# Kernel tuning notes

Hardware: AMD Instinct MI355X
Metric: run time of the kernel (lower is better)

## Reference

```python
import jax, jax.numpy as jnp
import numpy as np

OUTPUT_DIM = 512
INPUT_DIM = 64
BATCH = 131072


def setup_inputs() -> dict:
    key = jax.random.key(0)
    k1, k2, k3, k4 = jax.random.split(key, 4)
    D = INPUT_DIM + OUTPUT_DIM
    X = jax.random.normal(k1, (BATCH, OUTPUT_DIM), dtype=jnp.float32)
    c = jax.random.normal(k2, (BATCH, INPUT_DIM), dtype=jnp.float32)
    PA = jax.random.normal(k3, (OUTPUT_DIM, D), dtype=jnp.float32) * 0.05
    PB = jax.random.normal(k4, (OUTPUT_DIM, D), dtype=jnp.float32) * 0.05
    return {"X": X, "c": c, "PA": PA, "PB": PB}


def reference(X, c, PA, PB):
    # x = cat(c, X) : [B, D] with D = INPUT_DIM + OUTPUT_DIM
    x = jnp.concatenate([c, X], axis=1)
    D = INPUT_DIM + OUTPUT_DIM
    mask = (jnp.arange(D)[None, :] < (INPUT_DIM + jnp.arange(OUTPUT_DIM))[:, None]).astype(x.dtype)
    A = x @ (PA * mask).T  # [B, OUTPUT_DIM], A[:, i] = pa[i] @ x[:, :INPUT_DIM+i]
    Bv = x @ (PB * mask).T  # [B, OUTPUT_DIM]
    z = X * jnp.exp(A) + Bv  # [B, OUTPUT_DIM]
    log_det = jnp.sum(A, axis=1)  # [B]
    return z, log_det
```

## Files before the change

kernel.cpp:

```cpp
#include <hip/hip_runtime.h>
#include <hip/hip_bf16.h>
#include <stdint.h>

#define N_OUT 512
#define N_IN 64
#define D_TOT 576
#define BM 32
#define ROW_BYTES (D_TOT * 2)
#define NWAVES 4

typedef __attribute__((ext_vector_type(8))) short short8_t;
typedef __attribute__((ext_vector_type(4))) float f32x4;
typedef unsigned short u16;

__device__ __forceinline__ u16 f2bf(float f) {
    __hip_bfloat16 h = __float2bfloat16(f);
    return *reinterpret_cast<u16*>(&h);
}
__device__ __forceinline__ float bf2f(u16 u) {
    union { uint32_t u; float f; } v;
    v.u = ((uint32_t)u) << 16;
    return v.f;
}

__global__ void prep_weights_kernel(const float* __restrict__ PA,
                                    const float* __restrict__ PB,
                                    u16* __restrict__ WA,
                                    u16* __restrict__ WB) {
    const int col = blockIdx.x;
    const int lim = N_IN + col;
    const float* pa = PA + (size_t)col * D_TOT;
    const float* pb = PB + (size_t)col * D_TOT;
    for (int k = threadIdx.x; k < D_TOT; k += blockDim.x) {
        int kk = k >> 5, lg = (k >> 3) & 3, j = k & 7;
        size_t dst = ((size_t)(kk * 4 + lg) * N_OUT + col) * 8 + j;
        bool valid = (k < lim);
        WA[dst] = valid ? f2bf(pa[k]) : (u16)0;
        WB[dst] = valid ? f2bf(pb[k]) : (u16)0;
    }
}

__global__ __launch_bounds__(256)
void maf_main_kernel(const float* __restrict__ X,
                     const float* __restrict__ Cc,
                     const u16* __restrict__ WA,
                     const u16* __restrict__ WB,
                     float* __restrict__ Z,
                     float* __restrict__ LD) {
    extern __shared__ char smem[];
    char* xt = smem;
    float* ldsum = (float*)(smem + BM * ROW_BYTES);

    const int tid = threadIdx.x;
    const int r0 = blockIdx.x * BM;

    {
        int row = tid >> 3, cc = tid & 7;
        const float* src = Cc + (size_t)(r0 + row) * N_IN + cc * 8;
        f32x4 v0 = __builtin_nontemporal_load((const f32x4*)src);
        f32x4 v1 = __builtin_nontemporal_load((const f32x4*)(src + 4));
        short8_t p;
        p[0] = (short)f2bf(v0[0]); p[1] = (short)f2bf(v0[1]);
        p[2] = (short)f2bf(v0[2]); p[3] = (short)f2bf(v0[3]);
        p[4] = (short)f2bf(v1[0]); p[5] = (short)f2bf(v1[1]);
        p[6] = (short)f2bf(v1[2]); p[7] = (short)f2bf(v1[3]);
        int addr = (row * ROW_BYTES + cc * 16) ^ ((row & 7) << 4);
        *(short8_t*)(xt + addr) = p;
    }
    #pragma unroll
    for (int i = 0; i < 8; ++i) {
        int id = tid + i * 256;
        int row = id >> 6, xc = id & 63;
        const float* src = X + (size_t)(r0 + row) * N_OUT + xc * 8;
        f32x4 v0 = __builtin_nontemporal_load((const f32x4*)src);
        f32x4 v1 = __builtin_nontemporal_load((const f32x4*)(src + 4));
        short8_t p;
        p[0] = (short)f2bf(v0[0]); p[1] = (short)f2bf(v0[1]);
        p[2] = (short)f2bf(v0[2]); p[3] = (short)f2bf(v0[3]);
        p[4] = (short)f2bf(v1[0]); p[5] = (short)f2bf(v1[1]);
        p[6] = (short)f2bf(v1[2]); p[7] = (short)f2bf(v1[3]);
        int addr = (row * ROW_BYTES + (8 + xc) * 16) ^ ((row & 7) << 4);
        *(short8_t*)(xt + addr) = p;
    }
    __syncthreads();

    const int wid = tid >> 6;
    const int lane = tid & 63;
    const int lr = lane & 15;
    const int lg = lane >> 4;

    float part[2][4];
    #pragma unroll
    for (int m = 0; m < 2; ++m)
        #pragma unroll
        for (int j = 0; j < 4; ++j) part[m][j] = 0.0f;

    const int groups[4] = { wid, 7 - wid, 8 + wid, 15 - wid };

    #pragma unroll
    for (int gi = 0; gi < 4; ++gi) {
        const int g = groups[gi];
        const int c0 = g << 5;
        const int ksteps = 3 + g;

        f32x4 accA[2][2], accB[2][2];
        #pragma unroll
        for (int m = 0; m < 2; ++m)
            #pragma unroll
            for (int n = 0; n < 2; ++n) {
                accA[m][n] = (f32x4)(0.0f);
                accB[m][n] = (f32x4)(0.0f);
            }

        #pragma unroll 3
        for (int kk = 0; kk < ksteps; ++kk) {
            const int kb = kk * 64 + lg * 16;
            short8_t a[2];
            #pragma unroll
            for (int m = 0; m < 2; ++m) {
                int row = (m << 4) + lr;
                int addr = (row * ROW_BYTES + kb) ^ ((row & 7) << 4);
                a[m] = *(const short8_t*)(xt + addr);
            }
            short8_t ba[2], bb[2];
            const size_t wbase = (size_t)((kk << 2) + lg) * N_OUT + c0 + lr;
            #pragma unroll
            for (int n = 0; n < 2; ++n) {
                size_t off = (wbase + (n << 4)) * 8;
                ba[n] = *(const short8_t*)(WA + off);
                bb[n] = *(const short8_t*)(WB + off);
            }
            #pragma unroll
            for (int m = 0; m < 2; ++m) {
                #pragma unroll
                for (int n = 0; n < 2; ++n) {
                    accA[m][n] = __builtin_amdgcn_mfma_f32_16x16x32_bf16(a[m], ba[n], accA[m][n], 0, 0, 0);
                    accB[m][n] = __builtin_amdgcn_mfma_f32_16x16x32_bf16(a[m], bb[n], accB[m][n], 0, 0, 0);
                }
            }
        }

        #pragma unroll
        for (int m = 0; m < 2; ++m) {
            #pragma unroll
            for (int n = 0; n < 2; ++n) {
                int col = c0 + (n << 4) + lr;
                #pragma unroll
                for (int j = 0; j < 4; ++j) {
                    int row = (m << 4) + (lg << 2) + j;
                    float Av = accA[m][n][j];
                    float Bv = accB[m][n][j];
                    int xaddr = (row * ROW_BYTES + (N_IN + col) * 2) ^ ((row & 7) << 4);
                    float Xf = bf2f(*(const u16*)(xt + xaddr));
                    float zv = Xf * __expf(Av) + Bv;
                    __builtin_nontemporal_store(zv, &Z[(size_t)(r0 + row) * N_OUT + col]);
                    part[m][j] += Av;
                }
            }
        }
    }

    #pragma unroll
    for (int m = 0; m < 2; ++m) {
        #pragma unroll
        for (int j = 0; j < 4; ++j) {
            float v = part[m][j];
            v += __shfl_xor(v, 1);
            v += __shfl_xor(v, 2);
            v += __shfl_xor(v, 4);
            v += __shfl_xor(v, 8);
            if (lr == 0) ldsum[(wid << 5) + (m << 4) + (lg << 2) + j] = v;
        }
    }
    __syncthreads();
    if (tid < BM) {
        float s = 0.0f;
        #pragma unroll
        for (int w = 0; w < NWAVES; ++w) s += ldsum[(w << 5) + tid];
        LD[(size_t)r0 + tid] = s;
    }
}

extern "C" void kernel_launch(void* const* d_in, const int* in_sizes, int n_in,
                              void* d_out, int out_size, void* d_ws, size_t ws_size,
                              hipStream_t stream) {
    const float* X  = (const float*)d_in[0];
    const float* Cc = (const float*)d_in[1];
    const float* PA = (const float*)d_in[2];
    const float* PB = (const float*)d_in[3];

    u16* WA = (u16*)d_ws;
    u16* WB = WA + (size_t)N_OUT * D_TOT;

    float* Z  = (float*)d_out;
    const size_t batch = (size_t)in_sizes[0] / N_OUT;
    float* LD = Z + batch * N_OUT;

    prep_weights_kernel<<<N_OUT, 256, 0, stream>>>(PA, PB, WA, WB);

    const size_t lds_bytes = (size_t)BM * ROW_BYTES + NWAVES * BM * sizeof(float);
    const int grid = (int)(batch / BM);
    maf_main_kernel<<<grid, 256, lds_bytes, stream>>>(X, Cc, WA, WB, Z, LD);
}
```

Measured before the change: 216.4 us.

## Pair column groups per wave to share A-fragment loads across two MFMA chains

Each wave now processes two column groups at once (a short and a long triangular group), reusing the same LDS A-fragments across both groups during the shared k-steps and then finishing the longer group alone. This roughly halves LDS reads of the activation tile and gives more independent MFMA chains for latency hiding. It doubles accumulator register use, which may lower occupancy. The epilogue also switches from nontemporal stores to plain stores for Z.

```diff
diff --git a/kernel.cpp b/kernel.cpp
--- a/kernel.cpp
+++ b/kernel.cpp
@@ -40,6 +40,31 @@
     }
 }
 
+__device__ __forceinline__ void epilogue_group(const char* xt,
+                                               float* __restrict__ Z,
+                                               int r0, int c0, int lr, int lg,
+                                               const f32x4 accE[2][2],
+                                               const f32x4 accV[2][2],
+                                               float part[2][4]) {
+    #pragma unroll
+    for (int m = 0; m < 2; ++m) {
+        #pragma unroll
+        for (int n = 0; n < 2; ++n) {
+            int col = c0 + (n << 4) + lr;
+            #pragma unroll
+            for (int j = 0; j < 4; ++j) {
+                int row = (m << 4) + (lg << 2) + j;
+                float Av = accE[m][n][j];
+                float Bv = accV[m][n][j];
+                int xaddr = (row * ROW_BYTES + (N_IN + col) * 2) ^ ((row & 7) << 4);
+                float Xf = bf2f(*(const u16*)(xt + xaddr));
+                Z[(size_t)(r0 + row) * N_OUT + col] = Xf * __expf(Av) + Bv;
+                part[m][j] += Av;
+            }
+        }
+    }
+}
+
 __global__ __launch_bounds__(256)
 void maf_main_kernel(const float* __restrict__ X,
                      const float* __restrict__ Cc,
@@ -95,25 +120,27 @@
         #pragma unroll
         for (int j = 0; j < 4; ++j) part[m][j] = 0.0f;
 
-    const int groups[4] = { wid, 7 - wid, 8 + wid, 15 - wid };
-
-    #pragma unroll
-    for (int gi = 0; gi < 4; ++gi) {
-        const int g = groups[gi];
-        const int c0 = g << 5;
-        const int ksteps = 3 + g;
-
-        f32x4 accA[2][2], accB[2][2];
+    #pragma unroll
+    for (int pi = 0; pi < 2; ++pi) {
+        const int g0 = (pi == 0) ? wid : 7 - wid;
+        const int g1 = (pi == 0) ? 15 - wid : 8 + wid;
+        const int ks0 = 3 + g0;
+        const int ks1 = 3 + g1;
+        const int c00 = g0 << 5;
+        const int c01 = g1 << 5;
+
+        f32x4 accE0[2][2], accV0[2][2], accE1[2][2], accV1[2][2];
         #pragma unroll
         for (int m = 0; m < 2; ++m)
             #pragma unroll
             for (int n = 0; n < 2; ++n) {
-                accA[m][n] = (f32x4)(0.0f);
-                accB[m][n] = (f32x4)(0.0f);
-            }
-
-        #pragma unroll 3
-        for (int kk = 0; kk < ksteps; ++kk) {
+                accE0[m][n] = (f32x4)(0.0f); accV0[m][n] = (f32x4)(0.0f);
+                accE1[m][n] = (f32x4)(0.0f); accV1[m][n] = (f32x4)(0.0f);
+            }
+
+        int kk = 0;
+        #pragma unroll 2
+        for (; kk < ks0; ++kk) {
             const int kb = kk * 64 + lg * 16;
             short8_t a[2];
             #pragma unroll
@@ -122,42 +149,58 @@
                 int addr = (row * ROW_BYTES + kb) ^ ((row & 7) << 4);
                 a[m] = *(const short8_t*)(xt + addr);
             }
-            short8_t ba[2], bb[2];
-            const size_t wbase = (size_t)((kk << 2) + lg) * N_OUT + c0 + lr;
+            const size_t wrow = (size_t)((kk << 2) + lg) * N_OUT + lr;
+            short8_t e0[2], v0[2], e1[2], v1[2];
             #pragma unroll
             for (int n = 0; n < 2; ++n) {
-                size_t off = (wbase + (n << 4)) * 8;
-                ba[n] = *(const short8_t*)(WA + off);
-                bb[n] = *(const short8_t*)(WB + off);
+                size_t o0 = (wrow + c00 + (n << 4)) * 8;
+                size_t o1 = (wrow + c01 + (n << 4)) * 8;
+                e0[n] = *(const short8_t*)(WA + o0);
+                v0[n] = *(const short8_t*)(WB + o0);
+                e1[n] = *(const short8_t*)(WA + o1);
+                v1[n] = *(const short8_t*)(WB + o1);
             }
             #pragma unroll
             for (int m = 0; m < 2; ++m) {
                 #pragma unroll
                 for (int n = 0; n < 2; ++n) {
-                    accA[m][n] = __builtin_amdgcn_mfma_f32_16x16x32_bf16(a[m], ba[n], accA[m][n], 0, 0, 0);
-                    accB[m][n] = __builtin_amdgcn_mfma_f32_16x16x32_bf16(a[m], bb[n], accB[m][n], 0, 0, 0);
+                    accE0[m][n] = __builtin_amdgcn_mfma_f32_16x16x32_bf16(a[m], e0[n], accE0[m][n], 0, 0, 0);
+                    accV0[m][n] = __builtin_amdgcn_mfma_f32_16x16x32_bf16(a[m], v0[n], accV0[m][n], 0, 0, 0);
+                    accE1[m][n] = __builtin_amdgcn_mfma_f32_16x16x32_bf16(a[m], e1[n], accE1[m][n], 0, 0, 0);
+                    accV1[m][n] = __builtin_amdgcn_mfma_f32_16x16x32_bf16(a[m], v1[n], accV1[m][n], 0, 0, 0);
                 }
             }
         }
-
-        #pragma unroll
-        for (int m = 0; m < 2; ++m) {
+        #pragma unroll 2
+        for (; kk < ks1; ++kk) {
+            const int kb = kk * 64 + lg * 16;
+            short8_t a[2];
+            #pragma unroll
+            for (int m = 0; m < 2; ++m) {
+                int row = (m << 4) + lr;
+                int addr = (row * ROW_BYTES + kb) ^ ((row & 7) << 4);
+                a[m] = *(const short8_t*)(xt + addr);
+            }
+            const size_t wrow = (size_t)((kk << 2) + lg) * N_OUT + lr;
+            short8_t e1[2], v1[2];
             #pragma unroll
             for (int n = 0; n < 2; ++n) {
-                int col = c0 + (n << 4) + lr;
+                size_t o1 = (wrow + c01 + (n << 4)) * 8;
+                e1[n] = *(const short8_t*)(WA + o1);
+                v1[n] = *(const short8_t*)(WB + o1);
+            }
+            #pragma unroll
+            for (int m = 0; m < 2; ++m) {
                 #pragma unroll
-                for (int j = 0; j < 4; ++j) {
-                    int row = (m << 4) + (lg << 2) + j;
-                    float Av = accA[m][n][j];
-                    float Bv = accB[m][n][j];
-                    int xaddr = (row * ROW_BYTES + (N_IN + col) * 2) ^ ((row & 7) << 4);
-                    float Xf = bf2f(*(const u16*)(xt + xaddr));
-                    float zv = Xf * __expf(Av) + Bv;
-                    __builtin_nontemporal_store(zv, &Z[(size_t)(r0 + row) * N_OUT + col]);
-                    part[m][j] += Av;
+                for (int n = 0; n < 2; ++n) {
+                    accE1[m][n] = __builtin_amdgcn_mfma_f32_16x16x32_bf16(a[m], e1[n], accE1[m][n], 0, 0, 0);
+                    accV1[m][n] = __builtin_amdgcn_mfma_f32_16x16x32_bf16(a[m], v1[n], accV1[m][n], 0, 0, 0);
                 }
             }
         }
+
+        epilogue_group(xt, Z, r0, c00, lr, lg, accE0, accV0, part);
+        epilogue_group(xt, Z, r0, c01, lr, lg, accE1, accV1, part);
     }
 
     #pragma unroll
```

New measurement: 238.2 us. +10.1%, slower.

## Enlarge row tile to 128 with 1024-thread blocks and 32x32 MFMA

Applied to the files above, without the earlier changes.

Raises the batch tile from 32 to 128 rows, with 16 waves per block arranged as 4 row quarters by 4 column groups. The inner product moves from 16x16x32 to 32x32x16 bf16 MFMA, and the packed weight layout is simplified to match the new fragment shape. The aim is fewer, larger blocks and fewer MFMA instructions per tile. The cost is about 149 KB of LDS per block, which allows only one block per CU, so load and compute phases from different blocks no longer overlap. The Z stores also lose their nontemporal hint.

```diff
diff --git a/kernel.cpp b/kernel.cpp
--- a/kernel.cpp
+++ b/kernel.cpp
@@ -5,12 +5,14 @@
 #define N_OUT 512
 #define N_IN 64
 #define D_TOT 576
-#define BM 32
+#define BM 128
 #define ROW_BYTES (D_TOT * 2)
-#define NWAVES 4
+#define XT_BYTES (BM * ROW_BYTES)
+#define LDS_TOTAL (XT_BYTES + 4 * BM * 4)
 
 typedef __attribute__((ext_vector_type(8))) short short8_t;
 typedef __attribute__((ext_vector_type(4))) float f32x4;
+typedef __attribute__((ext_vector_type(16))) float f32x16;
 typedef unsigned short u16;
 
 __device__ __forceinline__ u16 f2bf(float f) {
@@ -32,15 +34,14 @@
     const float* pa = PA + (size_t)col * D_TOT;
     const float* pb = PB + (size_t)col * D_TOT;
     for (int k = threadIdx.x; k < D_TOT; k += blockDim.x) {
-        int kk = k >> 5, lg = (k >> 3) & 3, j = k & 7;
-        size_t dst = ((size_t)(kk * 4 + lg) * N_OUT + col) * 8 + j;
+        size_t dst = (size_t)(k >> 3) * (N_OUT * 8) + (size_t)col * 8 + (k & 7);
         bool valid = (k < lim);
         WA[dst] = valid ? f2bf(pa[k]) : (u16)0;
         WB[dst] = valid ? f2bf(pb[k]) : (u16)0;
     }
 }
 
-__global__ __launch_bounds__(256)
+__global__ __launch_bounds__(1024)
 void maf_main_kernel(const float* __restrict__ X,
                      const float* __restrict__ Cc,
                      const u16* __restrict__ WA,
@@ -49,7 +50,7 @@
                      float* __restrict__ LD) {
     extern __shared__ char smem[];
     char* xt = smem;
-    float* ldsum = (float*)(smem + BM * ROW_BYTES);
+    float* ldsum = (float*)(smem + XT_BYTES);
 
     const int tid = threadIdx.x;
     const int r0 = blockIdx.x * BM;
@@ -69,7 +70,7 @@
     }
     #pragma unroll
     for (int i = 0; i < 8; ++i) {
-        int id = tid + i * 256;
+        int id = tid + i * 1024;
         int row = id >> 6, xc = id & 63;
         const float* src = X + (size_t)(r0 + row) * N_OUT + xc * 8;
         f32x4 v0 = __builtin_nontemporal_load((const f32x4*)src);
@@ -84,100 +85,77 @@
     }
     __syncthreads();
 
-    const int wid = tid >> 6;
+    const int wid  = tid >> 6;
     const int lane = tid & 63;
-    const int lr = lane & 15;
-    const int lg = lane >> 4;
+    const int cw = wid & 3;
+    const int rq = wid >> 2;
+    const int cl = lane & 31;
+    const int hi = lane >> 5;
 
-    float part[2][4];
+    const int rowBase = (rq << 5) + cl;
+    const int aswz = (rowBase & 7) << 4;
+
+    float part[16];
     #pragma unroll
-    for (int m = 0; m < 2; ++m)
-        #pragma unroll
-        for (int j = 0; j < 4; ++j) part[m][j] = 0.0f;
-
-    const int groups[4] = { wid, 7 - wid, 8 + wid, 15 - wid };
+    for (int r = 0; r < 16; ++r) part[r] = 0.0f;
 
     #pragma unroll
     for (int gi = 0; gi < 4; ++gi) {
-        const int g = groups[gi];
-        const int c0 = g << 5;
-        const int ksteps = 3 + g;
+        const int g = (gi == 0) ? cw : (gi == 1) ? 7 - cw : (gi == 2) ? 8 + cw : 15 - cw;
+        const int ks = 3 + g;
+        const int gc = (g << 5) + cl;
 
-        f32x4 accA[2][2], accB[2][2];
-        #pragma unroll
-        for (int m = 0; m < 2; ++m)
-            #pragma unroll
-            for (int n = 0; n < 2; ++n) {
-                accA[m][n] = (f32x4)(0.0f);
-                accB[m][n] = (f32x4)(0.0f);
-            }
+        f32x16 aE = (f32x16)(0.0f);
+        f32x16 aV = (f32x16)(0.0f);
 
-        #pragma unroll 3
-        for (int kk = 0; kk < ksteps; ++kk) {
-            const int kb = kk * 64 + lg * 16;
-            short8_t a[2];
-            #pragma unroll
-            for (int m = 0; m < 2; ++m) {
-                int row = (m << 4) + lr;
-                int addr = (row * ROW_BYTES + kb) ^ ((row & 7) << 4);
-                a[m] = *(const short8_t*)(xt + addr);
-            }
-            short8_t ba[2], bb[2];
-            const size_t wbase = (size_t)((kk << 2) + lg) * N_OUT + c0 + lr;
-            #pragma unroll
-            for (int n = 0; n < 2; ++n) {
-                size_t off = (wbase + (n << 4)) * 8;
-                ba[n] = *(const short8_t*)(WA + off);
-                bb[n] = *(const short8_t*)(WB + off);
-            }
-            #pragma unroll
-            for (int m = 0; m < 2; ++m) {
-                #pragma unroll
-                for (int n = 0; n < 2; ++n) {
-                    accA[m][n] = __builtin_amdgcn_mfma_f32_16x16x32_bf16(a[m], ba[n], accA[m][n], 0, 0, 0);
-                    accB[m][n] = __builtin_amdgcn_mfma_f32_16x16x32_bf16(a[m], bb[n], accB[m][n], 0, 0, 0);
-                }
-            }
+        const u16* wa = WA + ((size_t)hi * N_OUT + gc) * 8;
+        const u16* wb = WB + ((size_t)hi * N_OUT + gc) * 8;
+
+        for (int kk = 0; kk < ks; ++kk) {
+            const int ab = rowBase * ROW_BYTES + kk * 64 + (hi << 4);
+            short8_t a0 = *(const short8_t*)(xt + (ab ^ aswz));
+            short8_t a1 = *(const short8_t*)(xt + ((ab + 32) ^ aswz));
+            const u16* wak = wa + (size_t)kk * 16384;
+            const u16* wbk = wb + (size_t)kk * 16384;
+            short8_t e0 = *(const short8_t*)(wak);
+            short8_t e1 = *(const short8_t*)(wak + 8192);
+            short8_t v0 = *(const short8_t*)(wbk);
+            short8_t v1 = *(const short8_t*)(wbk + 8192);
+            aE = __builtin_amdgcn_mfma_f32_32x32x16_bf16(a0, e0, aE, 0, 0, 0);
+            aE = __builtin_amdgcn_mfma_f32_32x32x16_bf16(a1, e1, aE, 0, 0, 0);
+            aV = __builtin_amdgcn_mfma_f32_32x32x16_bf16(a0, v0, aV, 0, 0, 0);
+            aV = __builtin_amdgcn_mfma_f32_32x32x16_bf16(a1, v1, aV, 0, 0, 0);
         }
 
         #pragma unroll
-        for (int m = 0; m < 2; ++m) {
-            #pragma unroll
-            for (int n = 0; n < 2; ++n) {
-                int col = c0 + (n << 4) + lr;
-                #pragma unroll
-                for (int j = 0; j < 4; ++j) {
-                    int row = (m << 4) + (lg << 2) + j;
-                    float Av = accA[m][n][j];
-                    float Bv = accB[m][n][j];
-                    int xaddr = (row * ROW_BYTES + (N_IN + col) * 2) ^ ((row & 7) << 4);
-                    float Xf = bf2f(*(const u16*)(xt + xaddr));
-                    float zv = Xf * __expf(Av) + Bv;
-                    __builtin_nontemporal_store(zv, &Z[(size_t)(r0 + row) * N_OUT + col]);
-                    part[m][j] += Av;
-                }
-            }
+        for (int r = 0; r < 16; ++r) {
+            int row = (rq << 5) + (r & 3) + ((r >> 2) << 3) + (hi << 2);
+            float Av = aE[r];
+            float Bv = aV[r];
+            int xb = (row * ROW_BYTES + (N_IN + gc) * 2) ^ ((row & 7) << 4);
+            float Xf = bf2f(*(const u16*)(xt + xb));
+            Z[(size_t)(r0 + row) * N_OUT + gc] = Xf * __expf(Av) + Bv;
+            part[r] += Av;
         }
     }
 
     #pragma unroll
-    for (int m = 0; m < 2; ++m) {
-        #pragma unroll
-        for (int j = 0; j < 4; ++j) {
-            float v = part[m][j];
-            v += __shfl_xor(v, 1);
-            v += __shfl_xor(v, 2);
-            v += __shfl_xor(v, 4);
-            v += __shfl_xor(v, 8);
-            if (lr == 0) ldsum[(wid << 5) + (m << 4) + (lg << 2) + j] = v;
+    for (int r = 0; r < 16; ++r) {
+        float v = part[r];
+        v += __shfl_xor(v, 1);
+        v += __shfl_xor(v, 2);
+        v += __shfl_xor(v, 4);
+        v += __shfl_xor(v, 8);
+        v += __shfl_xor(v, 16);
+        if (cl == 0) {
+            int row = (rq << 5) + (r & 3) + ((r >> 2) << 3) + (hi << 2);
+            ldsum[cw * BM + row] = v;
         }
     }
     __syncthreads();
     if (tid < BM) {
-        float s = 0.0f;
-        #pragma unroll
-        for (int w = 0; w < NWAVES; ++w) s += ldsum[(w << 5) + tid];
-        LD[(size_t)r0 + tid] = s;
+        LD[(size_t)r0 + tid] = ldsum[tid] + ldsum[BM + tid]
+                             + ldsum[2 * BM + tid] + ldsum[3 * BM + tid];
     }
 }
 
@@ -198,7 +176,9 @@
 
     prep_weights_kernel<<<N_OUT, 256, 0, stream>>>(PA, PB, WA, WB);
 
-    const size_t lds_bytes = (size_t)BM * ROW_BYTES + NWAVES * BM * sizeof(float);
+    (void)hipFuncSetAttribute((const void*)maf_main_kernel,
+                              hipFuncAttributeMaxDynamicSharedMemorySize,
+                              LDS_TOTAL);
     const int grid = (int)(batch / BM);
-    maf_main_kernel<<<grid, 256, lds_bytes, stream>>>(X, Cc, WA, WB, Z, LD);
+    maf_main_kernel<<<grid, 1024, LDS_TOTAL, stream>>>(X, Cc, WA, WB, Z, LD);
 }
```

After: 346.6 us. +60.2%, slower.

## Enlarge row tile to 128 with 8 waves splitting column groups in pairs

Applied to the files above, without the earlier changes.

Raises the block row tile from 32 to 128 rows and the block to 512 threads (8 waves). Each pair of waves shares a 32-row strip and splits the 16 column groups between them, so each weight fragment read from global/L2 is reused across more rows per block. The LDS tile grows to about 147 KB, with launch bounds asking for 2 blocks per CU, which limits occupancy. It also swaps the nontemporal Z stores for ordinary stores and raises the dynamic shared memory limit through a function attribute.

```diff
diff --git a/kernel.cpp b/kernel.cpp
--- a/kernel.cpp
+++ b/kernel.cpp
@@ -5,21 +5,23 @@
 #define N_OUT 512
 #define N_IN 64
 #define D_TOT 576
-#define BM 32
+#define BM 128
 #define ROW_BYTES (D_TOT * 2)
-#define NWAVES 4
+#define XT_BYTES (BM * ROW_BYTES)
+#define LDS_TOTAL (XT_BYTES + 8 * 32 * 4)
 
 typedef __attribute__((ext_vector_type(8))) short short8_t;
 typedef __attribute__((ext_vector_type(4))) float f32x4;
 typedef unsigned short u16;
+typedef unsigned int u32;
 
 __device__ __forceinline__ u16 f2bf(float f) {
     __hip_bfloat16 h = __float2bfloat16(f);
     return *reinterpret_cast<u16*>(&h);
 }
 __device__ __forceinline__ float bf2f(u16 u) {
-    union { uint32_t u; float f; } v;
-    v.u = ((uint32_t)u) << 16;
+    union { u32 u; float f; } v;
+    v.u = ((u32)u) << 16;
     return v.f;
 }
 
@@ -40,7 +42,7 @@
     }
 }
 
-__global__ __launch_bounds__(256)
+__global__ __launch_bounds__(512, 2)
 void maf_main_kernel(const float* __restrict__ X,
                      const float* __restrict__ Cc,
                      const u16* __restrict__ WA,
@@ -49,13 +51,15 @@
                      float* __restrict__ LD) {
     extern __shared__ char smem[];
     char* xt = smem;
-    float* ldsum = (float*)(smem + BM * ROW_BYTES);
+    float* lsum = (float*)(smem + XT_BYTES);
 
     const int tid = threadIdx.x;
     const int r0 = blockIdx.x * BM;
 
-    {
-        int row = tid >> 3, cc = tid & 7;
+    #pragma unroll
+    for (int i = 0; i < 2; ++i) {
+        int id = tid + i * 512;
+        int row = id >> 3, cc = id & 7;
         const float* src = Cc + (size_t)(r0 + row) * N_IN + cc * 8;
         f32x4 v0 = __builtin_nontemporal_load((const f32x4*)src);
         f32x4 v1 = __builtin_nontemporal_load((const f32x4*)(src + 4));
@@ -68,8 +72,8 @@
         *(short8_t*)(xt + addr) = p;
     }
     #pragma unroll
-    for (int i = 0; i < 8; ++i) {
-        int id = tid + i * 256;
+    for (int i = 0; i < 16; ++i) {
+        int id = tid + i * 512;
         int row = id >> 6, xc = id & 63;
         const float* src = X + (size_t)(r0 + row) * N_OUT + xc * 8;
         f32x4 v0 = __builtin_nontemporal_load((const f32x4*)src);
@@ -84,100 +88,97 @@
     }
     __syncthreads();
 
-    const int wid = tid >> 6;
+    const int wid  = tid >> 6;
     const int lane = tid & 63;
     const int lr = lane & 15;
     const int lg = lane >> 4;
+    const int p     = wid & 1;
+    const int strip = wid >> 1;
+    const int rbase = strip << 5;
 
     float part[2][4];
     #pragma unroll
-    for (int m = 0; m < 2; ++m)
-        #pragma unroll
-        for (int j = 0; j < 4; ++j) part[m][j] = 0.0f;
-
-    const int groups[4] = { wid, 7 - wid, 8 + wid, 15 - wid };
-
-    #pragma unroll
-    for (int gi = 0; gi < 4; ++gi) {
-        const int g = groups[gi];
+    for (int mm = 0; mm < 2; ++mm)
+        #pragma unroll
+        for (int j = 0; j < 4; ++j) part[mm][j] = 0.0f;
+
+    #pragma unroll
+    for (int gi = 0; gi < 8; ++gi) {
+        const int g = (gi << 1) + ((gi & 1) ? (1 - p) : p);
+        const int ks = 3 + g;
         const int c0 = g << 5;
-        const int ksteps = 3 + g;
-
-        f32x4 accA[2][2], accB[2][2];
-        #pragma unroll
-        for (int m = 0; m < 2; ++m)
+
+        f32x4 accE[2][2], accV[2][2];
+        #pragma unroll
+        for (int mm = 0; mm < 2; ++mm)
             #pragma unroll
             for (int n = 0; n < 2; ++n) {
-                accA[m][n] = (f32x4)(0.0f);
-                accB[m][n] = (f32x4)(0.0f);
-            }
-
-        #pragma unroll 3
-        for (int kk = 0; kk < ksteps; ++kk) {
-            const int kb = kk * 64 + lg * 16;
+                accE[mm][n] = (f32x4)(0.0f);
+                accV[mm][n] = (f32x4)(0.0f);
+            }
+
+        #pragma unroll 2
+        for (int kk = 0; kk < ks; ++kk) {
             short8_t a[2];
             #pragma unroll
-            for (int m = 0; m < 2; ++m) {
-                int row = (m << 4) + lr;
-                int addr = (row * ROW_BYTES + kb) ^ ((row & 7) << 4);
-                a[m] = *(const short8_t*)(xt + addr);
-            }
-            short8_t ba[2], bb[2];
+            for (int mm = 0; mm < 2; ++mm) {
+                int row = rbase + (mm << 4) + lr;
+                int addr = (row * ROW_BYTES + kk * 64 + (lg << 4)) ^ ((row & 7) << 4);
+                a[mm] = *(const short8_t*)(xt + addr);
+            }
+            short8_t bE[2], bV[2];
             const size_t wbase = (size_t)((kk << 2) + lg) * N_OUT + c0 + lr;
             #pragma unroll
             for (int n = 0; n < 2; ++n) {
                 size_t off = (wbase + (n << 4)) * 8;
-                ba[n] = *(const short8_t*)(WA + off);
-                bb[n] = *(const short8_t*)(WB + off);
-            }
-            #pragma unroll
-            for (int m = 0; m < 2; ++m) {
+                bE[n] = *(const short8_t*)(WA + off);
+                bV[n] = *(const short8_t*)(WB + off);
+            }
+            #pragma unroll
+            for (int mm = 0; mm < 2; ++mm) {
                 #pragma unroll
                 for (int n = 0; n < 2; ++n) {
-                    accA[m][n] = __builtin_amdgcn_mfma_f32_16x16x32_bf16(a[m], ba[n], accA[m][n], 0, 0, 0);
-                    accB[m][n] = __builtin_amdgcn_mfma_f32_16x16x32_bf16(a[m], bb[n], accB[m][n], 0, 0, 0);
+                    accE[mm][n] = __builtin_amdgcn_mfma_f32_16x16x32_bf16(a[mm], bE[n], accE[mm][n], 0, 0, 0);
+                    accV[mm][n] = __builtin_amdgcn_mfma_f32_16x16x32_bf16(a[mm], bV[n], accV[mm][n], 0, 0, 0);
                 }
             }
         }
 
         #pragma unroll
-        for (int m = 0; m < 2; ++m) {
+        for (int mm = 0; mm < 2; ++mm) {
             #pragma unroll
             for (int n = 0; n < 2; ++n) {
                 int col = c0 + (n << 4) + lr;
                 #pragma unroll
                 for (int j = 0; j < 4; ++j) {
-                    int row = (m << 4) + (lg << 2) + j;
-                    float Av = accA[m][n][j];
-                    float Bv = accB[m][n][j];
+                    int row = rbase + (mm << 4) + (lg << 2) + j;
+                    float Av = accE[mm][n][j];
+                    float Bv = accV[mm][n][j];
                     int xaddr = (row * ROW_BYTES + (N_IN + col) * 2) ^ ((row & 7) << 4);
                     float Xf = bf2f(*(const u16*)(xt + xaddr));
-                    float zv = Xf * __expf(Av) + Bv;
-                    __builtin_nontemporal_store(zv, &Z[(size_t)(r0 + row) * N_OUT + col]);
-                    part[m][j] += Av;
+                    Z[(size_t)(r0 + row) * N_OUT + col] = Xf * __expf(Av) + Bv;
+                    part[mm][j] += Av;
                 }
             }
         }
     }
 
     #pragma unroll
-    for (int m = 0; m < 2; ++m) {
+    for (int mm = 0; mm < 2; ++mm) {
         #pragma unroll
         for (int j = 0; j < 4; ++j) {
-            float v = part[m][j];
+            float v = part[mm][j];
             v += __shfl_xor(v, 1);
             v += __shfl_xor(v, 2);
             v += __shfl_xor(v, 4);
             v += __shfl_xor(v, 8);
-            if (lr == 0) ldsum[(wid << 5) + (m << 4) + (lg << 2) + j] = v;
+            if (lr == 0) lsum[(wid << 5) + (mm << 4) + (lg << 2) + j] = v;
         }
     }
     __syncthreads();
     if (tid < BM) {
-        float s = 0.0f;
-        #pragma unroll
-        for (int w = 0; w < NWAVES; ++w) s += ldsum[(w << 5) + tid];
-        LD[(size_t)r0 + tid] = s;
+        int sw = (tid >> 5) << 1, rloc = tid & 31;
+        LD[(size_t)r0 + tid] = lsum[(sw << 5) + rloc] + lsum[((sw + 1) << 5) + rloc];
     }
 }
 
@@ -198,7 +199,9 @@
 
     prep_weights_kernel<<<N_OUT, 256, 0, stream>>>(PA, PB, WA, WB);
 
-    const size_t lds_bytes = (size_t)BM * ROW_BYTES + NWAVES * BM * sizeof(float);
+    (void)hipFuncSetAttribute((const void*)maf_main_kernel,
+                              hipFuncAttributeMaxDynamicSharedMemorySize,
+                              LDS_TOTAL);
     const int grid = (int)(batch / BM);
-    maf_main_kernel<<<grid, 256, lds_bytes, stream>>>(X, Cc, WA, WB, Z, LD);
-}
+    maf_main_kernel<<<grid, 512, LDS_TOTAL, stream>>>(X, Cc, WA, WB, Z, LD);
+}
```

Measured after the change: 304.1 us. 40.6% more time.
